# Kernel tuning notes

Measured on AMD Instinct MI355X. Metric: run time of the kernel, lower is better.

## Reference

```python
import jax, jax.numpy as jnp
import numpy as np

N_LAYER = 3
N_HEAD = 12
D_K = 64
D_V = 64
D_MODEL = 768
D_INNER = 4096
LN_EPS = 1e-5
BN_EPS = 1e-5
PAD_ID = 1


def _layernorm(x, g, b):
    m = jnp.mean(x, axis=-1, keepdims=True)
    v = jnp.mean((x - m) ** 2, axis=-1, keepdims=True)
    return g * (x - m) / jnp.sqrt(v + LN_EPS) + b


def _batchnorm(x, g, b):
    # training-mode BatchNorm1d: per-feature batch statistics
    m = jnp.mean(x, axis=0)
    v = jnp.mean((x - m) ** 2, axis=0)
    return g * (x - m) / jnp.sqrt(v + BN_EPS) + b


def setup_inputs() -> dict:
    key = jax.random.key(0)
    ks = jax.random.split(key, 24)
    B, C, S, H = 4, 4, 256, D_MODEL
    inp = {
        'input_ids': jax.random.randint(ks[0], (B, C, S), 0, 50000, dtype=jnp.int64) if jax.config.read('jax_enable_x64') else jax.random.randint(ks[0], (B, C, S), 0, 50000, dtype=jnp.int32),
        'roberta_attn': jax.random.normal(ks[1], (B, C, S, H), dtype=jnp.float32),
        'pooled_output': jax.random.normal(ks[2], (B * C, H), dtype=jnp.float32),
        'commonsense_mask': jax.random.uniform(ks[3], (B, C, S, S), dtype=jnp.float32),
        'dependency_mask': jax.random.uniform(ks[4], (B, C, S, S), dtype=jnp.float32),
        'entity_mask': jax.random.uniform(ks[5], (B, C, S), dtype=jnp.float32),
        'sentiment_mask': jax.random.uniform(ks[6], (B, C, S, S), dtype=jnp.float32),
    }
    s = 0.02
    inp['lin_w'] = s * jax.random.normal(ks[7], (H, N_LAYER * 4), dtype=jnp.float32)
    inp['lin_b'] = jnp.zeros((N_LAYER * 4,), jnp.float32)
    inp['Wq'] = s * jax.random.normal(ks[8], (N_LAYER, H, N_HEAD * D_K), dtype=jnp.float32)
    inp['bq'] = jnp.zeros((N_LAYER, N_HEAD * D_K), jnp.float32)
    inp['Wk'] = s * jax.random.normal(ks[9], (N_LAYER, H, N_HEAD * D_K), dtype=jnp.float32)
    inp['bk'] = jnp.zeros((N_LAYER, N_HEAD * D_K), jnp.float32)
    inp['Wv'] = s * jax.random.normal(ks[10], (N_LAYER, H, N_HEAD * D_V), dtype=jnp.float32)
    inp['bv'] = jnp.zeros((N_LAYER, N_HEAD * D_V), jnp.float32)
    inp['Wo'] = s * jax.random.normal(ks[11], (N_LAYER, N_HEAD * D_V, H), dtype=jnp.float32)
    inp['bo'] = jnp.zeros((N_LAYER, H), jnp.float32)
    inp['ln1_g'] = jnp.ones((N_LAYER, H), jnp.float32)
    inp['ln1_b'] = jnp.zeros((N_LAYER, H), jnp.float32)
    inp['W1'] = s * jax.random.normal(ks[12], (N_LAYER, H, D_INNER), dtype=jnp.float32)
    inp['b1'] = jnp.zeros((N_LAYER, D_INNER), jnp.float32)
    inp['W2'] = s * jax.random.normal(ks[13], (N_LAYER, D_INNER, H), dtype=jnp.float32)
    inp['b2'] = jnp.zeros((N_LAYER, H), jnp.float32)
    inp['ln2_g'] = jnp.ones((N_LAYER, H), jnp.float32)
    inp['ln2_b'] = jnp.zeros((N_LAYER, H), jnp.float32)
    inp['bnt_g'] = jnp.ones((H,), jnp.float32)
    inp['bnt_b'] = jnp.zeros((H,), jnp.float32)
    inp['pool_w'] = s * jax.random.normal(ks[14], (H, H), dtype=jnp.float32)
    inp['pool_b'] = jnp.zeros((H,), jnp.float32)
    inp['bn_g'] = jnp.ones((H,), jnp.float32)
    inp['bn_b'] = jnp.zeros((H,), jnp.float32)
    inp['cls_w'] = s * jax.random.normal(ks[15], (H, 1), dtype=jnp.float32)
    inp['cls_b'] = jnp.zeros((1,), jnp.float32)
    return inp


def reference(input_ids, roberta_attn, pooled_output, commonsense_mask, dependency_mask,
              entity_mask, sentiment_mask, lin_w, lin_b, Wq, bq, Wk, bk, Wv, bv, Wo, bo,
              ln1_g, ln1_b, W1, b1, W2, b2, ln2_g, ln2_b, bnt_g, bnt_b,
              pool_w, pool_b, bn_g, bn_b, cls_w, cls_b):
    B, C, S = input_ids.shape
    H = roberta_attn.shape[-1]
    N = B * C
    x = roberta_attn.reshape(N, S, H)

    # learned softmax fusion weights over the 4 relational masks, per layer
    w = jnp.mean(x, axis=1) @ lin_w + lin_b                       # [N, 3*4]
    w = jax.nn.softmax(w.reshape(N, N_LAYER, 4).transpose(1, 0, 2), axis=-1)  # [3, N, 4]

    ent = jnp.broadcast_to(entity_mask[:, :, None, :], (B, C, S, S))
    masks = jnp.stack([
        commonsense_mask.reshape(N, S, S),
        dependency_mask.reshape(N, S, S),
        ent.reshape(N, S, S),
        sentiment_mask.reshape(N, S, S),
    ], axis=1)                                                     # [N, 4, S, S]
    bias = jnp.einsum('lnm,nmqk->lnqk', w, masks)                  # [3, N, S, S]

    non_pad = (input_ids.reshape(N, S) != PAD_ID).astype(x.dtype)[:, :, None]  # [N, S, 1]

    enc = x
    scale = 1.0 / np.sqrt(D_K).astype(np.float32)
    for l in range(N_LAYER):
        residual = enc
        q = (enc @ Wq[l] + bq[l]).reshape(N, S, N_HEAD, D_K)
        k = (enc @ Wk[l] + bk[l]).reshape(N, S, N_HEAD, D_K)
        v = (enc @ Wv[l] + bv[l]).reshape(N, S, N_HEAD, D_V)
        scores = jnp.einsum('nqhd,nkhd->nhqk', q, k) * scale + bias[l][:, None]  # [N,H,S,S]
        attn = jax.nn.softmax(scores, axis=-1)
        o = jnp.einsum('nhqk,nkhd->nqhd', attn, v).reshape(N, S, N_HEAD * D_V)
        o = o @ Wo[l] + bo[l]
        enc = _layernorm(o + residual, ln1_g[l], ln1_b[l]) * non_pad
        residual = enc
        f = jax.nn.relu(enc @ W1[l] + b1[l]) @ W2[l] + b2[l]
        enc = _layernorm(f + residual, ln2_g[l], ln2_b[l]) * non_pad

    enc = _batchnorm(enc.reshape(N * S, H), bnt_g, bnt_b).reshape(N, S, H)
    seq = x + enc
    pooled = jnp.tanh(seq[:, 0] @ pool_w + pool_b)
    pooled = _batchnorm(pooled, bn_g, bn_b)
    logits = pooled @ cls_w + cls_b                                # [N, 1]
    return logits.reshape(-1, C)
```

## Files before the change

kernel.cpp:

```cpp
#include <hip/hip_runtime.h>
#include <hip/hip_bf16.h>
#include <math.h>

#define NSEQ 16
#define SEQ 256
#define H 768
#define NH 12
#define DKH 64
#define DI 4096
#define MROWS (NSEQ*SEQ)
#define QKVN (3*H)

typedef __bf16 v8bf __attribute__((ext_vector_type(8)));
typedef float  v4f  __attribute__((ext_vector_type(4)));
typedef short  v8s  __attribute__((ext_vector_type(8)));

__device__ inline unsigned short bf16b(float f) {
  __hip_bfloat16 h = __float2bfloat16(f);
  return *reinterpret_cast<unsigned short*>(&h);
}
__device__ inline float b2f(unsigned short b) {
  return __uint_as_float(((unsigned int)b) << 16);
}

__device__ __forceinline__ void gload16(const void* g, void* l) {
  __builtin_amdgcn_global_load_lds((const __attribute__((address_space(1))) void*)g,
                                   (__attribute__((address_space(3))) void*)l, 16, 0, 0);
}

__device__ __forceinline__ void waitvm(int n) {
  switch (n) {
    case 0:  asm volatile("s_waitcnt vmcnt(0)" ::: "memory"); break;
    case 4:  asm volatile("s_waitcnt vmcnt(4)" ::: "memory"); break;
    case 8:  asm volatile("s_waitcnt vmcnt(8)" ::: "memory"); break;
    case 12: asm volatile("s_waitcnt vmcnt(12)" ::: "memory"); break;
    case 16: asm volatile("s_waitcnt vmcnt(16)" ::: "memory"); break;
    default: asm volatile("s_waitcnt vmcnt(0)" ::: "memory"); break;
  }
}

enum { MODE_F32_BIAS=0, MODE_BF16_BIAS=1, MODE_BF16_BIAS_RELU=2, MODE_SCORES=3, MODE_PV=4 };

template<int BM, int BN, int MODE, int DEPTH, bool SWZ>
__global__ __launch_bounds__(256) void k_mm(
    const unsigned short* __restrict__ A, int lda, long long saN, long long saH,
    const unsigned short* __restrict__ B, int ldb, long long sbN, long long sbH,
    void* __restrict__ Cout, int ldc, long long scN, long long scH,
    const float* __restrict__ bias, int K, int nhdiv) {
  constexpr int MI = BM/32, NI = BN/32;
  constexpr int AISS = BM/32, BISS = BN/32;
  constexpr int LPT = AISS + BISS;
  constexpr int TA = BM*64, TB = BN*64;
  __shared__ unsigned short As[DEPTH*TA];
  __shared__ unsigned short Bs[DEPTH*TB];
  int t = threadIdx.x;
  int z = blockIdx.z, n = z / nhdiv, h = z - n*nhdiv;
  int lane = t & 63, wid = t >> 6, wr = wid >> 1, wc = wid & 1;

  int bx = blockIdx.x, by = blockIdx.y;
  if (SWZ) {
    int gx = gridDim.x;
    int nwg = gx * gridDim.y;
    int lin = by*gx + bx;
    int q = nwg >> 3, r = nwg & 7;
    int xcd = lin & 7, idx = lin >> 3;
    int swz = (xcd < r) ? (xcd*(q+1) + idx) : (r*(q+1) + (xcd-r)*q + idx);
    bx = swz % gx; by = swz / gx;
  }

  const unsigned short* Ab = A + (size_t)n*saN + (size_t)h*saH + (size_t)by*BM*lda;
  const unsigned short* Bb = B + (size_t)n*sbN + (size_t)h*sbH + (size_t)bx*BN*ldb;

  const unsigned short* aSrc[AISS]; int aOff[AISS];
#pragma unroll
  for (int r = 0; r < AISS; ++r) {
    int chunk = wid*AISS + r;
    int row = chunk*8 + (lane >> 3);
    int col = ((lane & 7) ^ (row & 7)) * 8;
    aSrc[r] = Ab + (size_t)row*lda + col;
    aOff[r] = chunk*512;
  }
  const unsigned short* bSrc[BISS]; int bOff[BISS];
#pragma unroll
  for (int r = 0; r < BISS; ++r) {
    int chunk = wid*BISS + r;
    int row = chunk*8 + (lane >> 3);
    int col = ((lane & 7) ^ (row & 7)) * 8;
    bSrc[r] = Bb + (size_t)row*ldb + col;
    bOff[r] = chunk*512;
  }

  v4f acc[MI][NI];
#pragma unroll
  for (int i = 0; i < MI; ++i)
#pragma unroll
    for (int j = 0; j < NI; ++j) acc[i][j] = (v4f){0.f,0.f,0.f,0.f};

  auto issue = [&](int tt, int buf) {
    int k0 = tt << 6;
#pragma unroll
    for (int r = 0; r < AISS; ++r) gload16(aSrc[r] + k0, &As[buf*TA + aOff[r]]);
#pragma unroll
    for (int r = 0; r < BISS; ++r) gload16(bSrc[r] + k0, &Bs[buf*TB + bOff[r]]);
  };

  int nt = K >> 6;
  for (int p = 0; p < DEPTH-1 && p < nt; ++p) issue(p, p);
  int cbuf = 0;
  int ibuf = (DEPTH-1) % DEPTH;
  for (int tt = 0; tt < nt; ++tt) {
    int ahead = tt + DEPTH - 1;
    if (ahead < nt) {
      issue(ahead, ibuf);
      waitvm((DEPTH-1)*LPT);
    } else {
      waitvm((nt-1-tt)*LPT);
    }
    __builtin_amdgcn_s_barrier();
    asm volatile("" ::: "memory");
#pragma unroll
    for (int ks = 0; ks < 2; ++ks) {
      v8bf af[MI], bfr[NI];
#pragma unroll
      for (int i = 0; i < MI; ++i) {
        int row = wr*(BM/2) + i*16 + (lane & 15);
        int c = (ks*4 + (lane >> 4)) ^ (row & 7);
        af[i] = *(const v8bf*)&As[cbuf*TA + row*64 + c*8];
      }
#pragma unroll
      for (int j = 0; j < NI; ++j) {
        int row = wc*(BN/2) + j*16 + (lane & 15);
        int c = (ks*4 + (lane >> 4)) ^ (row & 7);
        bfr[j] = *(const v8bf*)&Bs[cbuf*TB + row*64 + c*8];
      }
#pragma unroll
      for (int i = 0; i < MI; ++i)
#pragma unroll
        for (int j = 0; j < NI; ++j)
          acc[i][j] = __builtin_amdgcn_mfma_f32_16x16x32_bf16(af[i], bfr[j], acc[i][j], 0, 0, 0);
    }
    asm volatile("s_waitcnt lgkmcnt(0)" ::: "memory");
    __builtin_amdgcn_s_barrier();
    asm volatile("" ::: "memory");
    cbuf = (cbuf + 1 == DEPTH) ? 0 : cbuf + 1;
    ibuf = (ibuf + 1 == DEPTH) ? 0 : ibuf + 1;
  }

  float* Cf = (float*)Cout;
  unsigned short* Ch = (unsigned short*)Cout;
  size_t cb = (size_t)n*scN + (size_t)h*scH;
  int grow0 = by*BM + wr*(BM/2);
  int gcol0 = bx*BN + wc*(BN/2);
#pragma unroll
  for (int i = 0; i < MI; ++i) {
#pragma unroll
    for (int j = 0; j < NI; ++j) {
      int col = gcol0 + j*16 + (lane & 15);
      float bval = 0.f;
      if (MODE == MODE_F32_BIAS || MODE == MODE_BF16_BIAS || MODE == MODE_BF16_BIAS_RELU)
        bval = bias[col];
#pragma unroll
      for (int r = 0; r < 4; ++r) {
        int row = grow0 + i*16 + (lane>>4)*4 + r;
        float v = acc[i][j][r];
        if (MODE == MODE_SCORES) {
          v = v*0.125f + bias[(size_t)n*65536 + (size_t)row*256 + col];
          Ch[cb + (size_t)row*ldc + col] = bf16b(v);
        } else if (MODE == MODE_F32_BIAS) {
          Cf[cb + (size_t)row*ldc + col] = v + bval;
        } else if (MODE == MODE_PV) {
          Ch[cb + (size_t)row*ldc + col] = bf16b(v);
        } else {
          v += bval;
          if (MODE == MODE_BF16_BIAS_RELU) v = fmaxf(v, 0.f);
          Ch[cb + (size_t)row*ldc + col] = bf16b(v);
        }
      }
    }
  }
}

__global__ __launch_bounds__(256) void k_wT(const float* __restrict__ in,
                                            unsigned short* __restrict__ out,
                                            int Nn, int Kk) {
  int n0 = blockIdx.x*64, k0 = blockIdx.y*64;
  __shared__ float T[64][72];
  int t = threadIdx.x;
  int r = t >> 4, c4 = (t & 15) * 4;
#pragma unroll
  for (int i = 0; i < 4; ++i) {
    float4 v = *(const float4*)(in + (size_t)(k0 + r + i*16)*Nn + n0 + c4);
    T[c4+0][r+i*16] = v.x; T[c4+1][r+i*16] = v.y;
    T[c4+2][r+i*16] = v.z; T[c4+3][r+i*16] = v.w;
  }
  __syncthreads();
  int c = t >> 3, r8 = (t & 7) * 8;
#pragma unroll
  for (int i = 0; i < 2; ++i) {
    int cc = c + i*32;
    v8s o;
#pragma unroll
    for (int j = 0; j < 8; ++j) o[j] = (short)bf16b(T[cc][r8+j]);
    *(v8s*)(out + (size_t)(n0+cc)*Kk + k0 + r8) = o;
  }
}

__global__ void k_bqkv(const float* __restrict__ bq, const float* __restrict__ bk,
                       const float* __restrict__ bv, float* __restrict__ o) {
  int i = blockIdx.x*256 + threadIdx.x;
  if (i >= 3*QKVN) return;
  int l = i / QKVN, j = i - l*QKVN;
  float v = (j < H) ? bq[l*H + j] : (j < 2*H) ? bk[l*H + j - H] : bv[l*H + j - 2*H];
  o[i] = v;
}

__global__ __launch_bounds__(256) void k_cast(const float* __restrict__ x,
                                              float* __restrict__ enc,
                                              unsigned short* __restrict__ enc16) {
  size_t i = ((size_t)blockIdx.x*256 + threadIdx.x)*4;
  float4 v = *(const float4*)(x + i);
  *(float4*)(enc + i) = v;
  ushort4 u = { bf16b(v.x), bf16b(v.y), bf16b(v.z), bf16b(v.w) };
  *(ushort4*)(enc16 + i) = u;
}

__global__ __launch_bounds__(256) void k_vT(const unsigned short* __restrict__ qkv,
                                            unsigned short* __restrict__ vT) {
  int z = blockIdx.x, n = z/NH, h = z - n*NH;
  const unsigned short* src = qkv + (size_t)n*SEQ*QKVN + 2*H + (size_t)h*DKH;
  __shared__ unsigned short tile[64][264];
  int t = threadIdx.x;
  int r0 = t >> 3, d0 = (t & 7) * 8;
#pragma unroll
  for (int i = 0; i < 8; ++i) {
    int r = r0 + i*32;
    v8s vv = *(const v8s*)(src + (size_t)r*QKVN + d0);
#pragma unroll
    for (int j = 0; j < 8; ++j) tile[d0+j][r] = (unsigned short)vv[j];
  }
  __syncthreads();
  int d = t >> 2, rb = (t & 3) * 64;
  unsigned short* dst = vT + (size_t)z*DKH*SEQ + (size_t)d*SEQ + rb;
#pragma unroll
  for (int i = 0; i < 8; ++i)
    *(v8s*)(dst + i*8) = *(const v8s*)&tile[d][rb + i*8];
}

__global__ __launch_bounds__(256) void k_fusion_weights(
    const float* __restrict__ x, const float* __restrict__ lin_w,
    const float* __restrict__ lin_b, float* __restrict__ wsoft) {
  int n = blockIdx.x, t = threadIdx.x;
  __shared__ float xm[H];
  __shared__ float sred[4];
  __shared__ float logits[12];
  if (t < 192) {
    const float4* p = (const float4*)(x + (size_t)n*SEQ*H) + t;
    float4 s = {0.f,0.f,0.f,0.f};
    for (int r = 0; r < SEQ; ++r) {
      float4 v = p[(size_t)r*192];
      s.x += v.x; s.y += v.y; s.z += v.z; s.w += v.w;
    }
    xm[t*4+0] = s.x*(1.0f/SEQ); xm[t*4+1] = s.y*(1.0f/SEQ);
    xm[t*4+2] = s.z*(1.0f/SEQ); xm[t*4+3] = s.w*(1.0f/SEQ);
  }
  __syncthreads();
  float lacc[12];
#pragma unroll
  for (int j = 0; j < 12; ++j) lacc[j] = 0.f;
  for (int hh = t; hh < H; hh += 256) {
    float xv = xm[hh];
#pragma unroll
    for (int j = 0; j < 12; ++j) lacc[j] += xv * lin_w[hh*12 + j];
  }
  for (int j = 0; j < 12; ++j) {
    float v = lacc[j];
#pragma unroll
    for (int m = 1; m < 64; m <<= 1) v += __shfl_xor(v, m, 64);
    if ((t & 63) == 0) sred[t >> 6] = v;
    __syncthreads();
    if (t == 0) logits[j] = sred[0]+sred[1]+sred[2]+sred[3] + lin_b[j];
    __syncthreads();
  }
  if (t < 3) {
    int l = t;
    float mx = -1e30f;
    for (int m = 0; m < 4; ++m) mx = fmaxf(mx, logits[l*4+m]);
    float e[4], s = 0.f;
    for (int m = 0; m < 4; ++m) { e[m] = expf(logits[l*4+m]-mx); s += e[m]; }
    for (int m = 0; m < 4; ++m) wsoft[(l*NSEQ + n)*4 + m] = e[m]/s;
  }
}

__global__ __launch_bounds__(256) void k_bias(
    const float* __restrict__ cm, const float* __restrict__ dm,
    const float* __restrict__ ent, const float* __restrict__ sm,
    const float* __restrict__ wsoft, int l, float* __restrict__ bias) {
  int g = blockIdx.x*256 + threadIdx.x;
  int n = g >> 14;
  int k4 = g & 63;
  const float* w = wsoft + (l*NSEQ + n)*4;
  float w0 = w[0], w1 = w[1], w2 = w[2], w3 = w[3];
  float4 c = ((const float4*)cm)[g];
  float4 d = ((const float4*)dm)[g];
  float4 s = ((const float4*)sm)[g];
  float4 e = ((const float4*)(ent + (size_t)n*SEQ))[k4];
  float4 o;
  o.x = w0*c.x + w1*d.x + w2*e.x + w3*s.x;
  o.y = w0*c.y + w1*d.y + w2*e.y + w3*s.y;
  o.z = w0*c.z + w1*d.z + w2*e.z + w3*s.z;
  o.w = w0*c.w + w1*d.w + w2*e.w + w3*s.w;
  ((float4*)bias)[g] = o;
}

__global__ void k_nonpad(const int* __restrict__ ids, float* __restrict__ npad) {
  int i = blockIdx.x*256 + threadIdx.x;
  if (i < MROWS) npad[i] = (ids[i] != 1) ? 1.0f : 0.0f;
}

__global__ __launch_bounds__(256) void k_softmax16(const unsigned short* __restrict__ s,
                                                   unsigned short* __restrict__ p) {
  int row = blockIdx.x*4 + (threadIdx.x >> 6);
  int lane = threadIdx.x & 63;
  ushort4 u = *(const ushort4*)(s + (size_t)row*SEQ + lane*4);
  float v0 = b2f(u.x), v1 = b2f(u.y), v2 = b2f(u.z), v3 = b2f(u.w);
  float mx = fmaxf(fmaxf(v0, v1), fmaxf(v2, v3));
#pragma unroll
  for (int m = 1; m < 64; m <<= 1) mx = fmaxf(mx, __shfl_xor(mx, m, 64));
  v0 = expf(v0-mx); v1 = expf(v1-mx); v2 = expf(v2-mx); v3 = expf(v3-mx);
  float sum = v0+v1+v2+v3;
#pragma unroll
  for (int m = 1; m < 64; m <<= 1) sum += __shfl_xor(sum, m, 64);
  float r = 1.0f/sum;
  ushort4 o = { bf16b(v0*r), bf16b(v1*r), bf16b(v2*r), bf16b(v3*r) };
  *(ushort4*)(p + (size_t)row*SEQ + lane*4) = o;
}

__global__ __launch_bounds__(256) void k_ln(
    const float* __restrict__ f, float* __restrict__ enc,
    unsigned short* __restrict__ enc16,
    const float* __restrict__ g, const float* __restrict__ b,
    const float* __restrict__ npad) {
  int r = blockIdx.x, t = threadIdx.x;
  size_t base = (size_t)r*H;
  float v0 = f[base+t]     + enc[base+t];
  float v1 = f[base+t+256] + enc[base+t+256];
  float v2 = f[base+t+512] + enc[base+t+512];
  __shared__ float sred[4];
  float s = v0+v1+v2;
#pragma unroll
  for (int m = 1; m < 64; m <<= 1) s += __shfl_xor(s, m, 64);
  if ((t & 63) == 0) sred[t >> 6] = s;
  __syncthreads();
  float mean = (sred[0]+sred[1]+sred[2]+sred[3]) * (1.0f/H);
  __syncthreads();
  float d0 = v0-mean, d1 = v1-mean, d2 = v2-mean;
  float ss = d0*d0 + d1*d1 + d2*d2;
#pragma unroll
  for (int m = 1; m < 64; m <<= 1) ss += __shfl_xor(ss, m, 64);
  if ((t & 63) == 0) sred[t >> 6] = ss;
  __syncthreads();
  float var = (sred[0]+sred[1]+sred[2]+sred[3]) * (1.0f/H);
  float rstd = 1.0f/sqrtf(var + 1e-5f);
  float npv = npad[r];
  float o0 = (g[t]    *d0*rstd + b[t]    )*npv;
  float o1 = (g[t+256]*d1*rstd + b[t+256])*npv;
  float o2 = (g[t+512]*d2*rstd + b[t+512])*npv;
  enc[base+t]     = o0; enc[base+t+256] = o1; enc[base+t+512] = o2;
  enc16[base+t]     = bf16b(o0);
  enc16[base+t+256] = bf16b(o1);
  enc16[base+t+512] = bf16b(o2);
}

__global__ __launch_bounds__(256) void k_colstats(
    const float* __restrict__ enc, float* __restrict__ csum, float* __restrict__ csq) {
  int r0 = blockIdx.x*64, t = threadIdx.x;
  float s0=0,s1=0,s2=0,q0=0,q1=0,q2=0;
  for (int r = 0; r < 64; ++r) {
    const float* row = enc + (size_t)(r0+r)*H;
    float a = row[t], b = row[t+256], c = row[t+512];
    s0 += a; s1 += b; s2 += c;
    q0 += a*a; q1 += b*b; q2 += c*c;
  }
  atomicAdd(&csum[t],     s0); atomicAdd(&csum[t+256], s1); atomicAdd(&csum[t+512], s2);
  atomicAdd(&csq[t],      q0); atomicAdd(&csq[t+256],  q1); atomicAdd(&csq[t+512],  q2);
}

__global__ __launch_bounds__(256) void k_poolprep(
    const float* __restrict__ x, const float* __restrict__ enc,
    const float* __restrict__ csum, const float* __restrict__ csq,
    const float* __restrict__ bnt_g, const float* __restrict__ bnt_b,
    float* __restrict__ ps0) {
  int n = blockIdx.x, t = threadIdx.x;
  for (int hh = t; hh < H; hh += 256) {
    float m = csum[hh] * (1.0f/MROWS);
    float var = csq[hh] * (1.0f/MROWS) - m*m;
    float rstd = 1.0f/sqrtf(var + 1e-5f);
    float e = enc[(size_t)n*SEQ*H + hh];
    ps0[n*H + hh] = x[(size_t)n*SEQ*H + hh] + bnt_g[hh]*(e-m)*rstd + bnt_b[hh];
  }
}

__global__ __launch_bounds__(256) void k_poolmm(
    const float* __restrict__ ps0, const float* __restrict__ pool_w,
    const float* __restrict__ pool_b, float* __restrict__ pooled) {
  int n = blockIdx.y, jb = blockIdx.x*64;
  __shared__ float s0[H];
  __shared__ float part[4][64];
  int t = threadIdx.x;
  for (int hh = t; hh < H; hh += 256) s0[hh] = ps0[n*H + hh];
  __syncthreads();
  int j = t & 63, q = t >> 6;
  float a = 0.f;
  int h0 = q*192;
  for (int hh = h0; hh < h0+192; ++hh)
    a = fmaf(s0[hh], pool_w[(size_t)hh*H + jb + j], a);
  part[q][j] = a;
  __syncthreads();
  if (t < 64) {
    float v = part[0][t]+part[1][t]+part[2][t]+part[3][t] + pool_b[jb+t];
    pooled[n*H + jb + t] = tanhf(v);
  }
}

__global__ __launch_bounds__(256) void k_final(
    const float* __restrict__ pooled, const float* __restrict__ bn_g,
    const float* __restrict__ bn_b, const float* __restrict__ cls_w,
    const float* __restrict__ cls_b, float* __restrict__ out) {
  int t = threadIdx.x;
  float acc[16];
#pragma unroll
  for (int n = 0; n < 16; ++n) acc[n] = 0.f;
  for (int hh = t; hh < H; hh += 256) {
    float p[16]; float m = 0.f;
#pragma unroll
    for (int n = 0; n < 16; ++n) { p[n] = pooled[n*H + hh]; m += p[n]; }
    m *= (1.0f/16.f);
    float var = 0.f;
#pragma unroll
    for (int n = 0; n < 16; ++n) { float d = p[n]-m; var += d*d; }
    var *= (1.0f/16.f);
    float rstd = 1.0f/sqrtf(var + 1e-5f);
    float gw = bn_g[hh]*rstd*cls_w[hh];
    float off = bn_b[hh]*cls_w[hh];
#pragma unroll
    for (int n = 0; n < 16; ++n) acc[n] += (p[n]-m)*gw + off;
  }
  __shared__ float sred[4];
  for (int n = 0; n < 16; ++n) {
    float v = acc[n];
#pragma unroll
    for (int m = 1; m < 64; m <<= 1) v += __shfl_xor(v, m, 64);
    if ((t & 63) == 0) sred[t >> 6] = v;
    __syncthreads();
    if (t == 0) out[n] = sred[0]+sred[1]+sred[2]+sred[3] + cls_b[0];
    __syncthreads();
  }
}

extern "C" void kernel_launch(void* const* d_in, const int* in_sizes, int n_in,
                              void* d_out, int out_size, void* d_ws, size_t ws_size,
                              hipStream_t stream) {
  const int*   input_ids = (const int*)  d_in[0];
  const float* x       = (const float*)d_in[1];
  const float* cm      = (const float*)d_in[3];
  const float* dm      = (const float*)d_in[4];
  const float* ent     = (const float*)d_in[5];
  const float* sm      = (const float*)d_in[6];
  const float* lin_w   = (const float*)d_in[7];
  const float* lin_b   = (const float*)d_in[8];
  const float* Wq      = (const float*)d_in[9];
  const float* bq      = (const float*)d_in[10];
  const float* Wk      = (const float*)d_in[11];
  const float* bk      = (const float*)d_in[12];
  const float* Wv      = (const float*)d_in[13];
  const float* bv      = (const float*)d_in[14];
  const float* Wo      = (const float*)d_in[15];
  const float* bo      = (const float*)d_in[16];
  const float* ln1_g   = (const float*)d_in[17];
  const float* ln1_b   = (const float*)d_in[18];
  const float* W1      = (const float*)d_in[19];
  const float* b1      = (const float*)d_in[20];
  const float* W2      = (const float*)d_in[21];
  const float* b2      = (const float*)d_in[22];
  const float* ln2_g   = (const float*)d_in[23];
  const float* ln2_b   = (const float*)d_in[24];
  const float* bnt_g   = (const float*)d_in[25];
  const float* bnt_b   = (const float*)d_in[26];
  const float* pool_w  = (const float*)d_in[27];
  const float* pool_b  = (const float*)d_in[28];
  const float* bn_g    = (const float*)d_in[29];
  const float* bn_b    = (const float*)d_in[30];
  const float* cls_w   = (const float*)d_in[31];
  const float* cls_b   = (const float*)d_in[32];
  float* out = (float*)d_out;
  (void)ws_size; (void)n_in; (void)in_sizes; (void)out_size;

  char* wsb = (char*)d_ws;
  size_t off = 0;
  auto alloc = [&](size_t bytes) {
    void* p = (void*)(wsb + off);
    off += (bytes + 255) & ~(size_t)255;
    return p;
  };
  float* enc            = (float*)alloc((size_t)MROWS*H*4);
  unsigned short* enc16 = (unsigned short*)alloc((size_t)MROWS*H*2);
  unsigned short* qkv16 = (unsigned short*)alloc((size_t)MROWS*QKVN*2);
  unsigned short* vT    = (unsigned short*)alloc((size_t)192*DKH*SEQ*2);
  unsigned short* ob16  = (unsigned short*)alloc((size_t)MROWS*H*2);
  float* fbuf           = (float*)alloc((size_t)MROWS*H*4);
  unsigned short* scoresB = (unsigned short*)alloc((size_t)MROWS*DI*2);
  unsigned short* hidden16 = scoresB;
  unsigned short* P16   = (unsigned short*)alloc((size_t)192*SEQ*SEQ*2);
  float* biasb          = (float*)alloc((size_t)NSEQ*SEQ*SEQ*4);
  unsigned short* WqkvT = (unsigned short*)alloc((size_t)3*QKVN*H*2);
  unsigned short* WoT   = (unsigned short*)alloc((size_t)3*H*H*2);
  unsigned short* W1T   = (unsigned short*)alloc((size_t)3*DI*H*2);
  unsigned short* W2T   = (unsigned short*)alloc((size_t)3*H*DI*2);
  float* bqkv   = (float*)alloc(3*QKVN*4);
  float* wsoft  = (float*)alloc(3*16*4*4);
  float* npad   = (float*)alloc(MROWS*4);
  float* csum   = (float*)alloc(H*4);
  float* csq    = (float*)alloc(H*4);
  float* ps0    = (float*)alloc(16*H*4);
  float* pooled = (float*)alloc(16*H*4);

  k_cast<<<MROWS*H/1024, 256, 0, stream>>>(x, enc, enc16);
  k_fusion_weights<<<16, 256, 0, stream>>>(x, lin_w, lin_b, wsoft);
  k_nonpad<<<MROWS/256, 256, 0, stream>>>(input_ids, npad);
  k_bqkv<<<27, 256, 0, stream>>>(bq, bk, bv, bqkv);
  for (int l = 0; l < 3; ++l) {
    k_wT<<<dim3(12,12), 256, 0, stream>>>(Wq + (size_t)l*H*H, WqkvT + (size_t)l*QKVN*H,           H, H);
    k_wT<<<dim3(12,12), 256, 0, stream>>>(Wk + (size_t)l*H*H, WqkvT + (size_t)l*QKVN*H + H*H,     H, H);
    k_wT<<<dim3(12,12), 256, 0, stream>>>(Wv + (size_t)l*H*H, WqkvT + (size_t)l*QKVN*H + 2*H*H,   H, H);
    k_wT<<<dim3(12,12), 256, 0, stream>>>(Wo + (size_t)l*H*H, WoT + (size_t)l*H*H,                H, H);
    k_wT<<<dim3(64,12), 256, 0, stream>>>(W1 + (size_t)l*H*DI, W1T + (size_t)l*DI*H,              DI, H);
    k_wT<<<dim3(12,64), 256, 0, stream>>>(W2 + (size_t)l*DI*H, W2T + (size_t)l*H*DI,              H, DI);
  }

  for (int l = 0; l < 3; ++l) {
    k_bias<<<1024, 256, 0, stream>>>(cm, dm, ent, sm, wsoft, l, biasb);
    k_mm<128,128,MODE_BF16_BIAS,1,true><<<dim3(18,32,1), 256, 0, stream>>>(
        enc16, H, 0, 0, WqkvT + (size_t)l*QKVN*H, H, 0, 0,
        qkv16, QKVN, 0, 0, bqkv + l*QKVN, H, 1);
    k_mm<64,64,MODE_SCORES,1,false><<<dim3(4,4,192), 256, 0, stream>>>(
        qkv16, QKVN, (long long)SEQ*QKVN, DKH,
        qkv16 + H, QKVN, (long long)SEQ*QKVN, DKH,
        scoresB, SEQ, (long long)NH*SEQ*SEQ, (long long)SEQ*SEQ,
        biasb, DKH, NH);
    k_softmax16<<<192*SEQ/4, 256, 0, stream>>>(scoresB, P16);
    k_vT<<<192, 256, 0, stream>>>(qkv16, vT);
    k_mm<64,64,MODE_PV,3,false><<<dim3(1,4,192), 256, 0, stream>>>(
        P16, SEQ, (long long)NH*SEQ*SEQ, (long long)SEQ*SEQ,
        vT, SEQ, (long long)NH*DKH*SEQ, (long long)DKH*SEQ,
        ob16, H, (long long)SEQ*H, DKH,
        nullptr, SEQ, NH);
    k_mm<64,64,MODE_F32_BIAS,3,true><<<dim3(12,64,1), 256, 0, stream>>>(
        ob16, H, 0, 0, WoT + (size_t)l*H*H, H, 0, 0,
        fbuf, H, 0, 0, bo + l*H, H, 1);
    k_ln<<<MROWS, 256, 0, stream>>>(fbuf, enc, enc16, ln1_g + l*H, ln1_b + l*H, npad);
    k_mm<128,128,MODE_BF16_BIAS_RELU,1,true><<<dim3(32,32,1), 256, 0, stream>>>(
        enc16, H, 0, 0, W1T + (size_t)l*DI*H, H, 0, 0,
        hidden16, DI, 0, 0, b1 + l*DI, H, 1);
    k_mm<64,64,MODE_F32_BIAS,3,true><<<dim3(12,64,1), 256, 0, stream>>>(
        hidden16, DI, 0, 0, W2T + (size_t)l*H*DI, DI, 0, 0,
        fbuf, H, 0, 0, b2 + l*H, DI, 1);
    k_ln<<<MROWS, 256, 0, stream>>>(fbuf, enc, enc16, ln2_g + l*H, ln2_b + l*H, npad);
  }

  hipMemsetAsync(csum, 0, H*sizeof(float), stream);
  hipMemsetAsync(csq,  0, H*sizeof(float), stream);
  k_colstats<<<64, 256, 0, stream>>>(enc, csum, csq);
  k_poolprep<<<16, 256, 0, stream>>>(x, enc, csum, csq, bnt_g, bnt_b, ps0);
  k_poolmm<<<dim3(12,16), 256, 0, stream>>>(ps0, pool_w, pool_b, pooled);
  k_final<<<1, 256, 0, stream>>>(pooled, bn_g, bn_b, cls_w, cls_b, out);
}
```

Before: 727.8 us.

## Fuse QK scores with softmax and split-K the FFN down-projection

```diff
diff --git a/kernel.cpp b/kernel.cpp
--- a/kernel.cpp
+++ b/kernel.cpp
@@ -39,7 +39,7 @@
   }
 }
 
-enum { MODE_F32_BIAS=0, MODE_BF16_BIAS=1, MODE_BF16_BIAS_RELU=2, MODE_SCORES=3, MODE_PV=4 };
+enum { MODE_F32_BIAS=0, MODE_BF16_BIAS=1, MODE_BF16_BIAS_RELU=2, MODE_SCORES=3, MODE_PV=4, MODE_F32_NOBIAS=5 };
 
 template<int BM, int BN, int MODE, int DEPTH, bool SWZ>
 __global__ __launch_bounds__(256) void k_mm(
@@ -168,6 +168,8 @@
           Ch[cb + (size_t)row*ldc + col] = bf16b(v);
         } else if (MODE == MODE_F32_BIAS) {
           Cf[cb + (size_t)row*ldc + col] = v + bval;
+        } else if (MODE == MODE_F32_NOBIAS) {
+          Cf[cb + (size_t)row*ldc + col] = v;
         } else if (MODE == MODE_PV) {
           Ch[cb + (size_t)row*ldc + col] = bf16b(v);
         } else {
@@ -177,6 +179,91 @@
         }
       }
     }
+  }
+}
+
+__global__ __launch_bounds__(256) void k_qksm(
+    const unsigned short* __restrict__ qkv,
+    const float* __restrict__ biasb,
+    unsigned short* __restrict__ P) {
+  __shared__ unsigned short Qs[64*64];
+  __shared__ unsigned short Ks[256*64];
+  int t = threadIdx.x, lane = t & 63, wid = t >> 6;
+  int z = blockIdx.y, n = z / NH, h = z - n*NH;
+  int m0 = blockIdx.x * 64;
+  const unsigned short* Qb = qkv + (size_t)n*SEQ*QKVN + (size_t)h*DKH + (size_t)m0*QKVN;
+  const unsigned short* Kb = qkv + (size_t)n*SEQ*QKVN + H + (size_t)h*DKH;
+#pragma unroll
+  for (int r = 0; r < 2; ++r) {
+    int chunk = wid*2 + r;
+    int row = chunk*8 + (lane >> 3);
+    int col = ((lane & 7) ^ (row & 7)) * 8;
+    gload16(Qb + (size_t)row*QKVN + col, &Qs[chunk*512]);
+  }
+#pragma unroll
+  for (int r = 0; r < 8; ++r) {
+    int chunk = wid*8 + r;
+    int row = chunk*8 + (lane >> 3);
+    int col = ((lane & 7) ^ (row & 7)) * 8;
+    gload16(Kb + (size_t)row*QKVN + col, &Ks[chunk*512]);
+  }
+  __syncthreads();
+  v4f acc[16];
+#pragma unroll
+  for (int j = 0; j < 16; ++j) acc[j] = (v4f){0.f,0.f,0.f,0.f};
+#pragma unroll
+  for (int ks = 0; ks < 2; ++ks) {
+    int arow = wid*16 + (lane & 15);
+    int ac = (ks*4 + (lane >> 4)) ^ (arow & 7);
+    v8bf af = *(const v8bf*)&Qs[arow*64 + ac*8];
+#pragma unroll
+    for (int j = 0; j < 16; ++j) {
+      int brow = j*16 + (lane & 15);
+      int bc = (ks*4 + (lane >> 4)) ^ (brow & 7);
+      v8bf bf = *(const v8bf*)&Ks[brow*64 + bc*8];
+      acc[j] = __builtin_amdgcn_mfma_f32_16x16x32_bf16(af, bf, acc[j], 0, 0, 0);
+    }
+  }
+  int col = lane & 15, quad = lane >> 4;
+  const float* bb = biasb + (size_t)n*65536;
+  float e[16][4];
+  float rm[4] = {-1e30f, -1e30f, -1e30f, -1e30f};
+#pragma unroll
+  for (int r = 0; r < 4; ++r) {
+    int row = m0 + wid*16 + quad*4 + r;
+#pragma unroll
+    for (int j = 0; j < 16; ++j) {
+      float v = acc[j][r]*0.125f + bb[(size_t)row*256 + j*16 + col];
+      e[j][r] = v;
+      rm[r] = fmaxf(rm[r], v);
+    }
+  }
+#pragma unroll
+  for (int r = 0; r < 4; ++r)
+#pragma unroll
+    for (int m = 1; m < 16; m <<= 1) rm[r] = fmaxf(rm[r], __shfl_xor(rm[r], m, 64));
+  float rs[4] = {0.f, 0.f, 0.f, 0.f};
+#pragma unroll
+  for (int r = 0; r < 4; ++r)
+#pragma unroll
+    for (int j = 0; j < 16; ++j) {
+      float ev = __expf(e[j][r] - rm[r]);
+      e[j][r] = ev;
+      rs[r] += ev;
+    }
+#pragma unroll
+  for (int r = 0; r < 4; ++r) {
+#pragma unroll
+    for (int m = 1; m < 16; m <<= 1) rs[r] += __shfl_xor(rs[r], m, 64);
+    rs[r] = 1.0f/rs[r];
+  }
+  unsigned short* Pz = P + (size_t)z*65536;
+#pragma unroll
+  for (int r = 0; r < 4; ++r) {
+    int row = m0 + wid*16 + quad*4 + r;
+#pragma unroll
+    for (int j = 0; j < 16; ++j)
+      Pz[(size_t)row*256 + j*16 + col] = bf16b(e[j][r]*rs[r]);
   }
 }
 
@@ -317,24 +404,6 @@
   if (i < MROWS) npad[i] = (ids[i] != 1) ? 1.0f : 0.0f;
 }
 
-__global__ __launch_bounds__(256) void k_softmax16(const unsigned short* __restrict__ s,
-                                                   unsigned short* __restrict__ p) {
-  int row = blockIdx.x*4 + (threadIdx.x >> 6);
-  int lane = threadIdx.x & 63;
-  ushort4 u = *(const ushort4*)(s + (size_t)row*SEQ + lane*4);
-  float v0 = b2f(u.x), v1 = b2f(u.y), v2 = b2f(u.z), v3 = b2f(u.w);
-  float mx = fmaxf(fmaxf(v0, v1), fmaxf(v2, v3));
-#pragma unroll
-  for (int m = 1; m < 64; m <<= 1) mx = fmaxf(mx, __shfl_xor(mx, m, 64));
-  v0 = expf(v0-mx); v1 = expf(v1-mx); v2 = expf(v2-mx); v3 = expf(v3-mx);
-  float sum = v0+v1+v2+v3;
-#pragma unroll
-  for (int m = 1; m < 64; m <<= 1) sum += __shfl_xor(sum, m, 64);
-  float r = 1.0f/sum;
-  ushort4 o = { bf16b(v0*r), bf16b(v1*r), bf16b(v2*r), bf16b(v3*r) };
-  *(ushort4*)(p + (size_t)row*SEQ + lane*4) = o;
-}
-
 __global__ __launch_bounds__(256) void k_ln(
     const float* __restrict__ f, float* __restrict__ enc,
     unsigned short* __restrict__ enc16,
@@ -345,6 +414,43 @@
   float v0 = f[base+t]     + enc[base+t];
   float v1 = f[base+t+256] + enc[base+t+256];
   float v2 = f[base+t+512] + enc[base+t+512];
+  __shared__ float sred[4];
+  float s = v0+v1+v2;
+#pragma unroll
+  for (int m = 1; m < 64; m <<= 1) s += __shfl_xor(s, m, 64);
+  if ((t & 63) == 0) sred[t >> 6] = s;
+  __syncthreads();
+  float mean = (sred[0]+sred[1]+sred[2]+sred[3]) * (1.0f/H);
+  __syncthreads();
+  float d0 = v0-mean, d1 = v1-mean, d2 = v2-mean;
+  float ss = d0*d0 + d1*d1 + d2*d2;
+#pragma unroll
+  for (int m = 1; m < 64; m <<= 1) ss += __shfl_xor(ss, m, 64);
+  if ((t & 63) == 0) sred[t >> 6] = ss;
+  __syncthreads();
+  float var = (sred[0]+sred[1]+sred[2]+sred[3]) * (1.0f/H);
+  float rstd = 1.0f/sqrtf(var + 1e-5f);
+  float npv = npad[r];
+  float o0 = (g[t]    *d0*rstd + b[t]    )*npv;
+  float o1 = (g[t+256]*d1*rstd + b[t+256])*npv;
+  float o2 = (g[t+512]*d2*rstd + b[t+512])*npv;
+  enc[base+t]     = o0; enc[base+t+256] = o1; enc[base+t+512] = o2;
+  enc16[base+t]     = bf16b(o0);
+  enc16[base+t+256] = bf16b(o1);
+  enc16[base+t+512] = bf16b(o2);
+}
+
+__global__ __launch_bounds__(256) void k_ln4(
+    const float* __restrict__ p, float* __restrict__ enc,
+    unsigned short* __restrict__ enc16,
+    const float* __restrict__ g, const float* __restrict__ b,
+    const float* __restrict__ npad, const float* __restrict__ cbias) {
+  int r = blockIdx.x, t = threadIdx.x;
+  size_t base = (size_t)r*H;
+  const size_t PS = (size_t)MROWS*H;
+  float v0 = p[base+t]     + p[PS+base+t]     + p[2*PS+base+t]     + p[3*PS+base+t]     + cbias[t]     + enc[base+t];
+  float v1 = p[base+t+256] + p[PS+base+t+256] + p[2*PS+base+t+256] + p[3*PS+base+t+256] + cbias[t+256] + enc[base+t+256];
+  float v2 = p[base+t+512] + p[PS+base+t+512] + p[2*PS+base+t+512] + p[3*PS+base+t+512] + cbias[t+512] + enc[base+t+512];
   __shared__ float sred[4];
   float s = v0+v1+v2;
 #pragma unroll
@@ -507,10 +613,10 @@
   unsigned short* qkv16 = (unsigned short*)alloc((size_t)MROWS*QKVN*2);
   unsigned short* vT    = (unsigned short*)alloc((size_t)192*DKH*SEQ*2);
   unsigned short* ob16  = (unsigned short*)alloc((size_t)MROWS*H*2);
-  float* fbuf           = (float*)alloc((size_t)MROWS*H*4);
-  unsigned short* scoresB = (unsigned short*)alloc((size_t)MROWS*DI*2);
-  unsigned short* hidden16 = scoresB;
-  unsigned short* P16   = (unsigned short*)alloc((size_t)192*SEQ*SEQ*2);
+  float* fbuf           = (float*)alloc((size_t)4*MROWS*H*4);
+  unsigned short* PH    = (unsigned short*)alloc((size_t)MROWS*DI*2);
+  unsigned short* P16     = PH;
+  unsigned short* hidden16 = PH;
   float* biasb          = (float*)alloc((size_t)NSEQ*SEQ*SEQ*4);
   unsigned short* WqkvT = (unsigned short*)alloc((size_t)3*QKVN*H*2);
   unsigned short* WoT   = (unsigned short*)alloc((size_t)3*H*H*2);
@@ -542,12 +648,7 @@
     k_mm<128,128,MODE_BF16_BIAS,1,true><<<dim3(18,32,1), 256, 0, stream>>>(
         enc16, H, 0, 0, WqkvT + (size_t)l*QKVN*H, H, 0, 0,
         qkv16, QKVN, 0, 0, bqkv + l*QKVN, H, 1);
-    k_mm<64,64,MODE_SCORES,1,false><<<dim3(4,4,192), 256, 0, stream>>>(
-        qkv16, QKVN, (long long)SEQ*QKVN, DKH,
-        qkv16 + H, QKVN, (long long)SEQ*QKVN, DKH,
-        scoresB, SEQ, (long long)NH*SEQ*SEQ, (long long)SEQ*SEQ,
-        biasb, DKH, NH);
-    k_softmax16<<<192*SEQ/4, 256, 0, stream>>>(scoresB, P16);
+    k_qksm<<<dim3(4,192), 256, 0, stream>>>(qkv16, biasb, P16);
     k_vT<<<192, 256, 0, stream>>>(qkv16, vT);
     k_mm<64,64,MODE_PV,3,false><<<dim3(1,4,192), 256, 0, stream>>>(
         P16, SEQ, (long long)NH*SEQ*SEQ, (long long)SEQ*SEQ,
@@ -561,10 +662,10 @@
     k_mm<128,128,MODE_BF16_BIAS_RELU,1,true><<<dim3(32,32,1), 256, 0, stream>>>(
         enc16, H, 0, 0, W1T + (size_t)l*DI*H, H, 0, 0,
         hidden16, DI, 0, 0, b1 + l*DI, H, 1);
-    k_mm<64,64,MODE_F32_BIAS,3,true><<<dim3(12,64,1), 256, 0, stream>>>(
-        hidden16, DI, 0, 0, W2T + (size_t)l*H*DI, DI, 0, 0,
-        fbuf, H, 0, 0, b2 + l*H, DI, 1);
-    k_ln<<<MROWS, 256, 0, stream>>>(fbuf, enc, enc16, ln2_g + l*H, ln2_b + l*H, npad);
+    k_mm<128,128,MODE_F32_NOBIAS,1,true><<<dim3(6,32,4), 256, 0, stream>>>(
+        hidden16, DI, 0, 1024, W2T + (size_t)l*H*DI, DI, 0, 1024,
+        fbuf, H, 0, (long long)MROWS*H, nullptr, 1024, 4);
+    k_ln4<<<MROWS, 256, 0, stream>>>(fbuf, enc, enc16, ln2_g + l*H, ln2_b + l*H, npad, b2 + l*H);
   }
 
   hipMemsetAsync(csum, 0, H*sizeof(float), stream);
```

New measurement: 696.4 us. 1.05x faster.
